# Optimization experiments

Measured on AMD Instinct MI355X. Metric: run time of the kernel, lower is better.

The kernel has to match this reference:

```python
import jax, jax.numpy as jnp
import numpy as np

B, K, T, D, NH, HD, DFF, L = 2, 512, 2048, 1024, 16, 64, 4096, 2
EPS = 1e-5


def rotate_half(x):
    x1, x2 = jnp.split(x, 2, axis=-1)
    return jnp.concatenate([-x2, x1], axis=-1)


def rmsnorm(x, w):
    return x * jax.lax.rsqrt(jnp.mean(x * x, axis=-1, keepdims=True) + EPS) * w


def setup_inputs():
    key = jax.random.key(0)
    ks = jax.random.split(key, 16)
    x_processed = jax.random.normal(ks[0], (B, K, D), jnp.float32)
    # counts[b] = number of chunks n; boundaries[b, :n-1] = ascending chunk ends in (0, T),
    # positions >= n-1 padded with T (sentinel, never used by the original loop).
    counts = jax.random.randint(ks[1], (B,), K // 2, K + 1)
    raw = jnp.sort(jax.random.randint(ks[2], (B, K), 1, T), axis=1)
    j = jnp.arange(K)[None, :]
    boundaries = jnp.where(j < counts[:, None] - 1, raw, T)
    x_residual = jax.random.normal(ks[3], (B, T, D), jnp.float32)
    inv_freq = 1.0 / (10000.0 ** (jnp.arange(0, HD, 2, dtype=jnp.float32) / HD))
    freqs = jnp.arange(T, dtype=jnp.float32)[:, None] * inv_freq[None, :]  # [T, HD//2]
    emb = jnp.concatenate([freqs, freqs], axis=-1)                          # [T, HD]
    cos, sin = jnp.cos(emb), jnp.sin(emb)
    s = 0.02
    wq = jax.random.normal(ks[4], (L, D, D), jnp.float32) * s
    wk = jax.random.normal(ks[5], (L, D, D), jnp.float32) * s
    wv = jax.random.normal(ks[6], (L, D, D), jnp.float32) * s
    wo = jax.random.normal(ks[7], (L, D, D), jnp.float32) * s
    w1 = jax.random.normal(ks[8], (L, D, DFF), jnp.float32) * s
    w3 = jax.random.normal(ks[9], (L, D, DFF), jnp.float32) * s
    w2 = jax.random.normal(ks[10], (L, DFF, D), jnp.float32) * s
    attn_norm_w = jnp.ones((L, D), jnp.float32)
    mlp_norm_w = jnp.ones((L, D), jnp.float32)
    final_norm_w = jnp.ones((D,), jnp.float32)
    return {"x_processed": x_processed, "boundaries": boundaries, "counts": counts,
            "x_residual": x_residual, "cos": cos, "sin": sin, "seq_len": T,
            "wq": wq, "wk": wk, "wv": wv, "wo": wo,
            "attn_norm_w": attn_norm_w, "mlp_norm_w": mlp_norm_w,
            "w1": w1, "w3": w3, "w2": w2, "final_norm_w": final_norm_w}


def reference(x_processed, boundaries, counts, x_residual, cos, sin, seq_len,
              wq, wk, wv, wo, attn_norm_w, mlp_norm_w, w1, w3, w2, final_norm_w):
    Bn, Kn, Dn = x_processed.shape
    Tn = x_residual.shape[1]
    # Vectorized chunk expansion: token t belongs to chunk i = #{boundaries <= t}
    # (boundaries ascending; entries beyond n-1 are padded with seq_len so they never count).
    t = jnp.arange(Tn)
    idx = jax.vmap(lambda row: jnp.searchsorted(row, t, side='right'))(boundaries)  # [B, T]
    x = jnp.take_along_axis(x_processed, idx[:, :, None], axis=1) + x_residual     # [B, T, D]

    mask = jnp.tril(jnp.ones((Tn, Tn), dtype=bool))
    scale = 1.0 / jnp.sqrt(jnp.float32(HD))
    c = cos[None, :, None, :]
    s = sin[None, :, None, :]
    for l in range(L):
        h = rmsnorm(x, attn_norm_w[l])
        q = (h @ wq[l]).reshape(Bn, Tn, NH, HD)
        k = (h @ wk[l]).reshape(Bn, Tn, NH, HD)
        v = (h @ wv[l]).reshape(Bn, Tn, NH, HD)
        q = q * c + rotate_half(q) * s
        k = k * c + rotate_half(k) * s
        scores = jnp.einsum('bthd,bshd->bhts', q, k) * scale
        scores = jnp.where(mask[None, None], scores, -jnp.inf)
        probs = jax.nn.softmax(scores, axis=-1)
        o = jnp.einsum('bhts,bshd->bthd', probs, v).reshape(Bn, Tn, Dn)
        x = x + o @ wo[l]
        h = rmsnorm(x, mlp_norm_w[l])
        x = x + (jax.nn.silu(h @ w1[l]) * (h @ w3[l])) @ w2[l]
    return rmsnorm(x, final_norm_w)
```

## Files before the change

kernel.cpp:

```cpp
#include <hip/hip_runtime.h>
#include <stdint.h>

typedef __attribute__((ext_vector_type(8))) short s16x8;
typedef __attribute__((ext_vector_type(4))) float f32x4;

#define CB 2
#define CT 2048
#define CD 1024
#define CNH 16
#define CHD 64
#define CDFF 4096
#define CKB 512

__device__ __forceinline__ short f2bf(float f){
  union { float f; uint32_t u; } v; v.f = f;
  uint32_t r = v.u + 0x7FFFu + ((v.u >> 16) & 1u);
  return (short)(r >> 16);
}
__device__ __forceinline__ float bf2f(short h){
  union { uint32_t u; float f; } v; v.u = ((uint32_t)(uint16_t)h) << 16;
  return v.f;
}
__device__ __forceinline__ uint32_t cvtpk_bf16(float lo, float hi){
  uint32_t r;
  asm("v_cvt_pk_bf16_f32 %0, %1, %2" : "=v"(r) : "v"(lo), "v"(hi));
  return r;
}

#define GLOAD16(g, l) __builtin_amdgcn_global_load_lds( \
    (const __attribute__((address_space(1))) void*)(g), \
    (__attribute__((address_space(3))) void*)(l), 16, 0, 0)

__global__ void gather_kernel(const float* __restrict__ xp, const int* __restrict__ bnd,
                              const float* __restrict__ xr, float* __restrict__ x){
  int t = blockIdx.x, b = blockIdx.y, tid = threadIdx.x;
  int lo = 0, hi = CKB;
  while (lo < hi){ int mid = (lo + hi) >> 1; if (bnd[b*CKB + mid] <= t) lo = mid + 1; else hi = mid; }
  const float4* s  = (const float4*)(xp + ((size_t)b*CKB + lo)*CD);
  const float4* rr = (const float4*)(xr + ((size_t)b*CT + t)*CD);
  float4* dst      = (float4*)(x  + ((size_t)b*CT + t)*CD);
  float4 a = s[tid], c = rr[tid];
  float4 o; o.x = a.x + c.x; o.y = a.y + c.y; o.z = a.z + c.z; o.w = a.w + c.w;
  dst[tid] = o;
}

__global__ void wtrans_kernel(const float* __restrict__ W, short* __restrict__ dst,
                              int Kd, int Nd){
  __shared__ __align__(16) float tile[64*65];
  int n0 = blockIdx.x*64, k0 = blockIdx.y*64;
  #pragma unroll
  for (int i = 0; i < 16; ++i){
    int e = threadIdx.x + 256*i; int kl = e >> 6, nl = e & 63;
    tile[kl*65 + nl] = W[(size_t)(k0 + kl)*Nd + n0 + nl];
  }
  __syncthreads();
  #pragma unroll
  for (int i = 0; i < 16; ++i){
    int e = threadIdx.x + 256*i; int nl = e >> 6, kl = e & 63;
    dst[(size_t)(n0 + nl)*Kd + k0 + kl] = f2bf(tile[kl*65 + nl]);
  }
}

__global__ void wtrans_inter_kernel(const float* __restrict__ W, short* __restrict__ dst,
                                    int Kd, int Nd, int off16){
  __shared__ __align__(16) float tile[64*65];
  int n0 = blockIdx.x*64, k0 = blockIdx.y*64;
  #pragma unroll
  for (int i = 0; i < 16; ++i){
    int e = threadIdx.x + 256*i; int kl = e >> 6, nl = e & 63;
    tile[kl*65 + nl] = W[(size_t)(k0 + kl)*Nd + n0 + nl];
  }
  __syncthreads();
  #pragma unroll
  for (int i = 0; i < 16; ++i){
    int e = threadIdx.x + 256*i; int nl = e >> 6, kl = e & 63;
    int c = n0 + nl;
    int frow = ((c >> 4) << 5) + off16 + (c & 15);
    dst[(size_t)frow*Kd + k0 + kl] = f2bf(tile[kl*65 + nl]);
  }
}

template<int OUT_BF16>
__global__ void rmsnorm_kernel(const float* __restrict__ x, const float* __restrict__ w,
                               void* __restrict__ outv){
  int row = blockIdx.x, tid = threadIdx.x;
  const float4 xv = ((const float4*)(x + (size_t)row*CD))[tid];
  float ss = xv.x*xv.x + xv.y*xv.y + xv.z*xv.z + xv.w*xv.w;
  #pragma unroll
  for (int m = 1; m < 64; m <<= 1) ss += __shfl_xor(ss, m);
  __shared__ float red[4];
  if ((tid & 63) == 0) red[tid >> 6] = ss;
  __syncthreads();
  float tot = red[0] + red[1] + red[2] + red[3];
  float scale = rsqrtf(tot * (1.0f/1024.0f) + 1e-5f);
  const float4 wv = ((const float4*)w)[tid];
  if (OUT_BF16){
    short4 o;
    o.x = f2bf(xv.x*scale*wv.x); o.y = f2bf(xv.y*scale*wv.y);
    o.z = f2bf(xv.z*scale*wv.z); o.w = f2bf(xv.w*scale*wv.w);
    ((short4*)outv)[(size_t)row*256 + tid] = o;
  } else {
    float4 o;
    o.x = xv.x*scale*wv.x; o.y = xv.y*scale*wv.y;
    o.z = xv.z*scale*wv.z; o.w = xv.w*scale*wv.w;
    ((float4*)outv)[(size_t)row*256 + tid] = o;
  }
}

template<int OUT_BF16>
__global__ void redrms_kernel(float* __restrict__ x, const float* __restrict__ Cp,
                              const float* __restrict__ w, void* __restrict__ outv){
  int row = blockIdx.x, tid = threadIdx.x;
  size_t i = (size_t)row*256 + tid;
  const float4* p0 = (const float4*)Cp;
  const float4* p1 = p0 + (size_t)1048576;
  const float4* p2 = p1 + (size_t)1048576;
  const float4* p3 = p2 + (size_t)1048576;
  float4 a = ((float4*)x)[i];
  float4 q0 = p0[i], q1 = p1[i], q2 = p2[i], q3 = p3[i];
  a.x += (q0.x + q1.x) + (q2.x + q3.x);
  a.y += (q0.y + q1.y) + (q2.y + q3.y);
  a.z += (q0.z + q1.z) + (q2.z + q3.z);
  a.w += (q0.w + q1.w) + (q2.w + q3.w);
  if (OUT_BF16) ((float4*)x)[i] = a;
  float ss = a.x*a.x + a.y*a.y + a.z*a.z + a.w*a.w;
  #pragma unroll
  for (int m = 1; m < 64; m <<= 1) ss += __shfl_xor(ss, m);
  __shared__ float red[4];
  if ((tid & 63) == 0) red[tid >> 6] = ss;
  __syncthreads();
  float tot = red[0] + red[1] + red[2] + red[3];
  float scale = rsqrtf(tot * (1.0f/1024.0f) + 1e-5f);
  const float4 wv = ((const float4*)w)[tid];
  if (OUT_BF16){
    short4 o;
    o.x = f2bf(a.x*scale*wv.x); o.y = f2bf(a.y*scale*wv.y);
    o.z = f2bf(a.z*scale*wv.z); o.w = f2bf(a.w*scale*wv.w);
    ((short4*)outv)[(size_t)row*256 + tid] = o;
  } else {
    float4 o;
    o.x = a.x*scale*wv.x; o.y = a.y*scale*wv.y;
    o.z = a.z*scale*wv.z; o.w = a.w*scale*wv.w;
    ((float4*)outv)[(size_t)row*256 + tid] = o;
  }
}

__device__ __forceinline__ void swz_block_id(int id, int NX, int NY, int& bm, int& bn){
  const int nwg = NX*NY;
  const int qq = nwg >> 3, rr8 = nwg & 7;
  const int xcd = id & 7, loc = id >> 3;
  const int wgid = (xcd < rr8 ? xcd*(qq+1) : rr8*(qq+1) + (xcd-rr8)*qq) + loc;
  const int GM = 8;
  const int gsz = GM * NX;
  const int gidg = wgid / gsz;
  const int remg = wgid - gidg*gsz;
  bm = gidg*GM + (remg % GM);
  bn = remg / GM;
}

template<int EPI>
__global__ __launch_bounds__(256) void gemm_bt(const short* __restrict__ A,
                                               const short* __restrict__ Bt,
                                               void* __restrict__ Cv,
                                               int M, int N, int K,
                                               int NX, int NY){
  __shared__ __align__(16) short sA[2][128*32];
  __shared__ __align__(16) short sB[2][128*32];
  const int tid = threadIdx.x;
  const int lane = tid & 63, wid = tid >> 6;
  const int wm = wid >> 1, wn = wid & 1;
  const int lr = lane & 15, lg = lane >> 4;
  int bm, bn; swz_block_id(blockIdx.x, NX, NY, bm, bn);
  const int bm0 = bm * 128, bn0 = bn * 128;

  f32x4 acc[4][4];
  #pragma unroll
  for (int i = 0; i < 4; ++i)
    #pragma unroll
    for (int j = 0; j < 4; ++j) acc[i][j] = (f32x4){0.f,0.f,0.f,0.f};

  const short* gA = A  + (size_t)(bm0 + wid*32 + (lane >> 2))*K + (lane & 3)*8;
  const short* gB = Bt + (size_t)(bn0 + wid*32 + (lane >> 2))*K + (lane & 3)*8;

  #pragma unroll
  for (int iss = 0; iss < 2; ++iss){
    GLOAD16(gA + (size_t)iss*16*K, &sA[0][wid*1024 + iss*16*32]);
    GLOAD16(gB + (size_t)iss*16*K, &sB[0][wid*1024 + iss*16*32]);
  }
  __syncthreads();

  int cur = 0;
  for (int k0 = 0; k0 < K; k0 += 32){
    if (k0 + 32 < K){
      #pragma unroll
      for (int iss = 0; iss < 2; ++iss){
        GLOAD16(gA + (size_t)iss*16*K + k0 + 32, &sA[cur^1][wid*1024 + iss*16*32]);
        GLOAD16(gB + (size_t)iss*16*K + k0 + 32, &sB[cur^1][wid*1024 + iss*16*32]);
      }
    }
    s16x8 af[4], bq[4];
    #pragma unroll
    for (int i = 0; i < 4; ++i) af[i] = *(const s16x8*)&sA[cur][(wm*64 + i*16 + lr)*32 + lg*8];
    #pragma unroll
    for (int j = 0; j < 4; ++j) bq[j] = *(const s16x8*)&sB[cur][(wn*64 + j*16 + lr)*32 + lg*8];
    #pragma unroll
    for (int i = 0; i < 4; ++i)
      #pragma unroll
      for (int j = 0; j < 4; ++j)
        acc[i][j] = __builtin_amdgcn_mfma_f32_16x16x32_bf16(af[i], bq[j], acc[i][j], 0, 0, 0);
    __syncthreads();
    cur ^= 1;
  }

  if (EPI == 0){
    short* C = (short*)Cv;
    #pragma unroll
    for (int i = 0; i < 4; ++i){
      int row0 = bm0 + wm*64 + i*16 + lg*4;
      #pragma unroll
      for (int j = 0; j < 4; ++j){
        int col = bn0 + wn*64 + j*16 + lr;
        #pragma unroll
        for (int r = 0; r < 4; ++r) C[(size_t)(row0 + r)*N + col] = f2bf(acc[i][j][r]);
      }
    }
  } else {
    float* C = (float*)Cv;
    #pragma unroll
    for (int i = 0; i < 4; ++i){
      int row0 = bm0 + wm*64 + i*16 + lg*4;
      #pragma unroll
      for (int j = 0; j < 4; ++j){
        int col = bn0 + wn*64 + j*16 + lr;
        #pragma unroll
        for (int r = 0; r < 4; ++r) C[(size_t)(row0 + r)*N + col] += acc[i][j][r];
      }
    }
  }
}

#define STAGE8(u, kt, bufx) do { \
  const short* Gp_ = ((u)&1) ? Bt : A; \
  const int rb_ = ((u)&1) ? bn0 : bm0; \
  const int kh_ = (u)>>1; \
  _Pragma("unroll") \
  for (int L_ = 0; L_ < 2; ++L_){ \
    int rowS_ = L_*128 + wid*16 + (lane>>2); \
    int sp_ = (lane&3) ^ ((rowS_>>1)&3); \
    GLOAD16(Gp_ + (size_t)(rb_ + rowS_)*Kstr + (size_t)(kt)*64 + kh_*32 + sp_*8, \
            &sAB[bufx][u][(L_*512 + wid*64)*8]); \
  } \
} while(0)

#define LDSRD(bufx, u, rowv) \
  (*(const s16x8*)&sAB[bufx][u][(rowv)*32 + (((lg) ^ (((rowv)>>1)&3))<<3)])

#define PHASEPAIR(kk) do { \
  if (pf){ STAGE8(2*(kk), kt+1, nbuf); STAGE8(2*(kk)+1, kt+1, nbuf); } \
  s16x8 af0_[4], af1_[4], bq_[4]; \
  _Pragma("unroll") \
  for (int j_ = 0; j_ < 4; ++j_) bq_[j_] = LDSRD(buf, (kk)*2+1, wn*64 + j_*16 + lr); \
  _Pragma("unroll") \
  for (int i_ = 0; i_ < 4; ++i_) af0_[i_] = LDSRD(buf, (kk)*2, wm*128 + i_*16 + lr); \
  _Pragma("unroll") \
  for (int i_ = 0; i_ < 4; ++i_) af1_[i_] = LDSRD(buf, (kk)*2, wm*128 + 64 + i_*16 + lr); \
  __builtin_amdgcn_s_barrier(); \
  asm volatile("s_waitcnt lgkmcnt(0)" ::: "memory"); \
  __builtin_amdgcn_s_setprio(1); \
  _Pragma("unroll") \
  for (int i_ = 0; i_ < 4; ++i_) \
    _Pragma("unroll") \
    for (int j_ = 0; j_ < 4; ++j_) \
      acc[i_][j_] = __builtin_amdgcn_mfma_f32_16x16x32_bf16(af0_[i_], bq_[j_], acc[i_][j_], 0, 0, 0); \
  _Pragma("unroll") \
  for (int i_ = 0; i_ < 4; ++i_) \
    _Pragma("unroll") \
    for (int j_ = 0; j_ < 4; ++j_) \
      acc[4+i_][j_] = __builtin_amdgcn_mfma_f32_16x16x32_bf16(af1_[i_], bq_[j_], acc[4+i_][j_], 0, 0, 0); \
  __builtin_amdgcn_s_setprio(0); \
  if (pf) asm volatile("s_waitcnt vmcnt(4)" ::: "memory"); \
  else if ((kk) == 0) asm volatile("s_waitcnt vmcnt(0)" ::: "memory"); \
  __builtin_amdgcn_s_barrier(); \
} while(0)

template<int FUSE>
__global__ __launch_bounds__(512, 2) void gemm8p(const short* __restrict__ A,
                                                 const short* __restrict__ Bt,
                                                 void* __restrict__ Cv,
                                                 short* __restrict__ Qo,
                                                 short* __restrict__ Ko,
                                                 short* __restrict__ Vo,
                                                 const float* __restrict__ cosb,
                                                 const float* __restrict__ sinb,
                                                 int M, int N, int Kstr, int Kchunk,
                                                 int NX, int NY){
  __shared__ __align__(16) short sAB[2][4][256*32];
  const int tid = threadIdx.x;
  const int lane = tid & 63, wid = tid >> 6;
  const int wm = wid >> 2, wn = wid & 3;
  const int lr = lane & 15, lg = lane >> 4;
  const int nin = NX*NY;
  const int split = blockIdx.x / nin;
  const int inner = blockIdx.x - split*nin;
  int bm, bn; swz_block_id(inner, NX, NY, bm, bn);
  const int bm0 = bm * 256, bn0 = bn * 256;
  A  += (size_t)split * Kchunk;
  Bt += (size_t)split * Kchunk;

  f32x4 acc[8][4];
  #pragma unroll
  for (int i = 0; i < 8; ++i)
    #pragma unroll
    for (int j = 0; j < 4; ++j) acc[i][j] = (f32x4){0.f,0.f,0.f,0.f};

  const int NK = Kchunk >> 6;
  STAGE8(0, 0, 0);
  STAGE8(1, 0, 0);
  STAGE8(2, 0, 0);
  STAGE8(3, 0, 0);
  asm volatile("s_waitcnt vmcnt(4)" ::: "memory");
  __builtin_amdgcn_s_barrier();

  #pragma unroll 1
  for (int kt = 0; kt < NK; ++kt){
    const bool pf = (kt + 1 < NK);
    const int buf = kt & 1, nbuf = buf ^ 1;
    PHASEPAIR(0);
    PHASEPAIR(1);
  }

  if (FUSE == 0){
    short* C = (short*)Cv;
    #pragma unroll
    for (int i = 0; i < 8; ++i){
      int row0 = bm0 + wm*128 + i*16 + lg*4;
      #pragma unroll
      for (int j = 0; j < 4; ++j){
        int col = bn0 + wn*64 + j*16 + lr;
        #pragma unroll
        for (int r = 0; r < 4; ++r) C[(size_t)(row0 + r)*N + col] = f2bf(acc[i][j][r]);
      }
    }
  } else if (FUSE == 1){
    short* C = (short*)Cv;
    const int Nh = N >> 1;
    #pragma unroll
    for (int i = 0; i < 8; ++i){
      int row0 = bm0 + wm*128 + i*16 + lg*4;
      #pragma unroll
      for (int jp = 0; jp < 2; ++jp){
        int col = (bn0 >> 1) + wn*32 + jp*16 + lr;
        #pragma unroll
        for (int r = 0; r < 4; ++r){
          float u = acc[i][jp*2][r], g = acc[i][jp*2+1][r];
          float val = u / (1.f + __expf(-u)) * g;
          C[(size_t)(row0 + r)*Nh + col] = f2bf(val);
        }
      }
    }
  } else if (FUSE == 2){
    float* C = (float*)Cv + (size_t)split*M*N;
    #pragma unroll
    for (int i = 0; i < 8; ++i){
      int row0 = bm0 + wm*128 + i*16 + lg*4;
      #pragma unroll
      for (int j = 0; j < 4; ++j){
        int col = bn0 + wn*64 + j*16 + lr;
        #pragma unroll
        for (int r = 0; r < 4; ++r) C[(size_t)(row0 + r)*N + col] = acc[i][j][r];
      }
    }
  } else {
    const int part = bn0 >> 10;
    const int colb = bn0 & 1023;
    const int h = (colb + wn*64) >> 6;
    if (part < 2){
      short* dst = (part == 0) ? Qo : Ko;
      const float qs = (part == 0) ? 0.1803368801111204f : 1.0f;
      #pragma unroll
      for (int i = 0; i < 8; ++i){
        int row0 = bm0 + wm*128 + i*16 + lg*4;
        #pragma unroll
        for (int jh = 0; jh < 2; ++jh){
          int d = jh*16 + lr;
          #pragma unroll
          for (int r = 0; r < 4; ++r){
            int tg = row0 + r;
            int bb = tg >> 11, tt = tg & 2047;
            float c = cosb[tt*64 + d], s = sinb[tt*64 + d];
            float x0 = acc[i][jh][r], x1 = acc[i][jh+2][r];
            float y0 = (x0*c - x1*s)*qs;
            float y1 = (x1*c + x0*s)*qs;
            size_t o = ((size_t)(bb*CT + tt)*CNH + h)*CHD;
            dst[o + d]      = f2bf(y0);
            dst[o + d + 32] = f2bf(y1);
          }
        }
      }
    } else {
      #pragma unroll
      for (int i = 0; i < 8; ++i){
        int row0 = bm0 + wm*128 + i*16 + lg*4;
        int bb = row0 >> 11, t0 = row0 & 2047;
        #pragma unroll
        for (int j = 0; j < 4; ++j){
          int d = j*16 + lr;
          short4 pk;
          pk.x = f2bf(acc[i][j][0]); pk.y = f2bf(acc[i][j][1]);
          pk.z = f2bf(acc[i][j][2]); pk.w = f2bf(acc[i][j][3]);
          *(short4*)&Vo[((size_t)(bb*CNH + h)*CHD + d)*CT + t0] = pk;
        }
      }
    }
  }
}

__global__ __launch_bounds__(256) void attn_kernel(const short* __restrict__ Q,
                                                   const short* __restrict__ Kb,
                                                   const short* __restrict__ Vt,
                                                   short* __restrict__ O){
  __shared__ __align__(16) short Kl[2][64*72];
  __shared__ __align__(16) short Vl[2][64*72];
  __shared__ __align__(16) short Pl[4][16*72];
  const int tid = threadIdx.x, lane = tid & 63, w = tid >> 6;
  const int qpair = blockIdx.x;
  const int h = blockIdx.y, b = blockIdx.z;
  const int lr = lane & 15, lg = lane >> 4;

  const short* gK = Kb + (size_t)b*CT*CD + h*CHD;
  const short* gV = Vt + (size_t)(b*CNH + h)*CHD*CT;
  const int srow0 = tid >> 3, scol = (tid & 7)*8;

  #pragma unroll 1
  for (int half = 0; half < 2; ++half){
    const int qt = half ? qpair : (31 - qpair);
    const int wq0 = qt*64 + w*16;
    const int jmax = qt + 1;

    s16x8 qf0, qf1;
    {
      const short* qp = Q + ((size_t)(b*CT + wq0 + lr)*CNH + h)*CHD + lg*8;
      qf0 = *(const s16x8*)qp;
      qf1 = *(const s16x8*)(qp + 32);
    }
    f32x4 oacc[4];
    #pragma unroll
    for (int dt = 0; dt < 4; ++dt) oacc[dt] = (f32x4){0.f,0.f,0.f,0.f};
    float m_r = -1e30f, l_r = 0.f;

    #pragma unroll
    for (int p = 0; p < 2; ++p){
      int row = srow0 + p*32;
      *(s16x8*)&Kl[0][row*72 + scol] = *(const s16x8*)(gK + (size_t)row*CD + scol);
      *(s16x8*)&Vl[0][row*72 + scol] = *(const s16x8*)(gV + (size_t)row*CT + scol);
    }
    __syncthreads();

    #pragma unroll 1
    for (int j = 0; j < jmax; ++j){
      const int kv0 = j*64;
      const int buf = j & 1;
      s16x8 nk[2], nv[2];
      const bool havenext = (j + 1 < jmax);
      if (havenext){
        const int kv1 = kv0 + 64;
        #pragma unroll
        for (int p = 0; p < 2; ++p){
          int row = srow0 + p*32;
          nk[p] = *(const s16x8*)(gK + (size_t)(kv1 + row)*CD + scol);
          nv[p] = *(const s16x8*)(gV + (size_t)row*CT + kv1 + scol);
        }
      }

      if (kv0 < wq0 + 16){
        f32x4 sc[4];
        __builtin_amdgcn_s_setprio(1);
        #pragma unroll
        for (int nt = 0; nt < 4; ++nt){
          s16x8 k0 = *(const s16x8*)&Kl[buf][(nt*16 + lr)*72 + lg*8];
          s16x8 k1 = *(const s16x8*)&Kl[buf][(nt*16 + lr)*72 + 32 + lg*8];
          f32x4 z = (f32x4){0.f,0.f,0.f,0.f};
          z = __builtin_amdgcn_mfma_f32_16x16x32_bf16(k0, qf0, z, 0, 0, 0);
          z = __builtin_amdgcn_mfma_f32_16x16x32_bf16(k1, qf1, z, 0, 0, 0);
          sc[nt] = z;
        }
        __builtin_amdgcn_s_setprio(0);
        if (kv0 + 64 > wq0){
          #pragma unroll
          for (int nt = 0; nt < 4; ++nt)
            #pragma unroll
            for (int r = 0; r < 4; ++r)
              if (kv0 + nt*16 + lg*4 + r > wq0 + lr) sc[nt][r] = -1e30f;
        }
        float pmax = sc[0][0];
        #pragma unroll
        for (int nt = 0; nt < 4; ++nt)
          #pragma unroll
          for (int r = 0; r < 4; ++r) pmax = fmaxf(pmax, sc[nt][r]);
        pmax = fmaxf(pmax, __shfl_xor(pmax, 16));
        pmax = fmaxf(pmax, __shfl_xor(pmax, 32));
        if (!__all(pmax - m_r <= 10.f)){
          float mn = fmaxf(m_r, pmax);
          float corr = __builtin_amdgcn_exp2f(m_r - mn);
          m_r = mn;
          l_r *= corr;
          #pragma unroll
          for (int r = 0; r < 4; ++r){
            float c4 = __shfl(corr, lg*4 + r);
            #pragma unroll
            for (int dt = 0; dt < 4; ++dt) oacc[dt][r] *= c4;
          }
        }
        float rs = 0.f;
        #pragma unroll
        for (int nt = 0; nt < 4; ++nt)
          #pragma unroll
          for (int r = 0; r < 4; ++r){
            float pv = __builtin_amdgcn_exp2f(sc[nt][r] - m_r);
            sc[nt][r] = pv;
            rs += pv;
          }
        #pragma unroll
        for (int nt = 0; nt < 4; ++nt){
          uint2 pk;
          pk.x = cvtpk_bf16(sc[nt][0], sc[nt][1]);
          pk.y = cvtpk_bf16(sc[nt][2], sc[nt][3]);
          *(uint2*)&Pl[w][lr*72 + nt*16 + lg*4] = pk;
        }
        rs += __shfl_xor(rs, 16);
        rs += __shfl_xor(rs, 32);
        l_r += rs;
        s16x8 pa0 = *(const s16x8*)&Pl[w][lr*72 + lg*8];
        s16x8 pa1 = *(const s16x8*)&Pl[w][lr*72 + 32 + lg*8];
        __builtin_amdgcn_s_setprio(1);
        #pragma unroll
        for (int dt = 0; dt < 4; ++dt){
          s16x8 v0 = *(const s16x8*)&Vl[buf][(dt*16 + lr)*72 + lg*8];
          s16x8 v1 = *(const s16x8*)&Vl[buf][(dt*16 + lr)*72 + 32 + lg*8];
          oacc[dt] = __builtin_amdgcn_mfma_f32_16x16x32_bf16(pa0, v0, oacc[dt], 0, 0, 0);
          oacc[dt] = __builtin_amdgcn_mfma_f32_16x16x32_bf16(pa1, v1, oacc[dt], 0, 0, 0);
        }
        __builtin_amdgcn_s_setprio(0);
      }
      if (havenext){
        #pragma unroll
        for (int p = 0; p < 2; ++p){
          int row = srow0 + p*32;
          *(s16x8*)&Kl[buf^1][row*72 + scol] = nk[p];
          *(s16x8*)&Vl[buf^1][row*72 + scol] = nv[p];
        }
      }
      __syncthreads();
    }

    #pragma unroll
    for (int r = 0; r < 4; ++r){
      float lf = __shfl(l_r, lg*4 + r);
      float inv = 1.f / lf;
      int qrow = wq0 + lg*4 + r;
      #pragma unroll
      for (int dt = 0; dt < 4; ++dt)
        O[((size_t)(b*CT + qrow)*CNH + h)*CHD + dt*16 + lr] = f2bf(oacc[dt][r] * inv);
    }
  }
}

extern "C" void kernel_launch(void* const* d_in, const int* in_sizes, int n_in,
                              void* d_out, int out_size, void* d_ws, size_t ws_size,
                              hipStream_t stream){
  (void)in_sizes; (void)n_in; (void)out_size; (void)ws_size;
  const float* x_processed = (const float*)d_in[0];
  const int*   boundaries  = (const int*)d_in[1];
  const float* x_residual  = (const float*)d_in[3];
  const float* cosb        = (const float*)d_in[4];
  const float* sinb        = (const float*)d_in[5];
  const float* wq          = (const float*)d_in[7];
  const float* wk          = (const float*)d_in[8];
  const float* wv          = (const float*)d_in[9];
  const float* wo          = (const float*)d_in[10];
  const float* attn_nw     = (const float*)d_in[11];
  const float* mlp_nw      = (const float*)d_in[12];
  const float* w1          = (const float*)d_in[13];
  const float* w3          = (const float*)d_in[14];
  const float* w2          = (const float*)d_in[15];
  const float* final_nw    = (const float*)d_in[16];

  char* p = (char*)d_ws;
  auto alloc = [&](size_t bytes)->char*{
    char* r = p; p += (bytes + 255) & ~(size_t)255; return r;
  };
  short* wqkvT = (short*)alloc((size_t)2*3072*1024*2);
  short* woT   = (short*)alloc((size_t)2*1024*1024*2);
  short* w13T  = (short*)alloc((size_t)2*8192*1024*2);
  short* w2T   = (short*)alloc((size_t)2*1024*4096*2);
  float* x     = (float*)alloc((size_t)4096*1024*4);
  short* hbuf  = (short*)alloc((size_t)4096*1024*2);
  short* qr    = (short*)alloc((size_t)4096*1024*2);
  short* kr    = (short*)alloc((size_t)4096*1024*2);
  short* vt    = (short*)alloc((size_t)4096*1024*2);
  short* obuf  = (short*)alloc((size_t)4096*1024*2);
  short* mbuf  = (short*)alloc((size_t)4096*4096*2);
  float* psum  = (float*)alloc((size_t)4*4096*1024*4);

  for (int l = 0; l < 2; ++l){
    size_t wOff = (size_t)l*1024*1024;
    wtrans_kernel<<<dim3(16,16),256,0,stream>>>(wq + wOff, wqkvT + (size_t)l*3072*1024,                     1024, 1024);
    wtrans_kernel<<<dim3(16,16),256,0,stream>>>(wk + wOff, wqkvT + (size_t)l*3072*1024 + (size_t)1024*1024, 1024, 1024);
    wtrans_kernel<<<dim3(16,16),256,0,stream>>>(wv + wOff, wqkvT + (size_t)l*3072*1024 + (size_t)2048*1024, 1024, 1024);
    wtrans_kernel<<<dim3(16,16),256,0,stream>>>(wo + wOff, woT + (size_t)l*1024*1024,                       1024, 1024);
    wtrans_inter_kernel<<<dim3(64,16),256,0,stream>>>(w1 + (size_t)l*1024*4096, w13T + (size_t)l*8192*1024, 1024, 4096, 0);
    wtrans_inter_kernel<<<dim3(64,16),256,0,stream>>>(w3 + (size_t)l*1024*4096, w13T + (size_t)l*8192*1024, 1024, 4096, 16);
    wtrans_kernel<<<dim3(16,64),256,0,stream>>>(w2 + (size_t)l*4096*1024, w2T + (size_t)l*1024*4096,        4096, 1024);
  }
  gather_kernel<<<dim3(2048,2),256,0,stream>>>(x_processed, boundaries, x_residual, x);
  rmsnorm_kernel<1><<<4096,256,0,stream>>>(x, attn_nw, hbuf);
  for (int l = 0; l < 2; ++l){
    gemm8p<3><<<12*16,512,0,stream>>>(hbuf, wqkvT + (size_t)l*3072*1024, nullptr,
                                      qr, kr, vt, cosb, sinb,
                                      4096, 3072, 1024, 1024, 12, 16);
    attn_kernel<<<dim3(16,16,2),256,0,stream>>>(qr, kr, vt, obuf);
    gemm_bt<1><<<8*32,256,0,stream>>>(obuf, woT + (size_t)l*1024*1024, x, 4096, 1024, 1024, 8, 32);
    rmsnorm_kernel<1><<<4096,256,0,stream>>>(x, mlp_nw + l*1024, hbuf);
    gemm8p<1><<<32*16,512,0,stream>>>(hbuf, w13T + (size_t)l*8192*1024, mbuf,
                                      nullptr, nullptr, nullptr, nullptr, nullptr,
                                      4096, 8192, 1024, 1024, 32, 16);
    gemm8p<2><<<4*4*16,512,0,stream>>>(mbuf, w2T + (size_t)l*1024*4096, psum,
                                       nullptr, nullptr, nullptr, nullptr, nullptr,
                                       4096, 1024, 4096, 1024, 4, 16);
    if (l == 0) redrms_kernel<1><<<4096,256,0,stream>>>(x, psum, attn_nw + 1024, hbuf);
    else        redrms_kernel<0><<<4096,256,0,stream>>>(x, psum, final_nw, d_out);
  }
}
```

Measured before the change: 607.6 us.

## Deepen gemm8p prefetch to two k-tiles and merge weight-transpose launches

The main GEMM loop is reorganized into four quarter-phases that issue global-to-LDS loads two k-tiles ahead instead of one. It reuses the A fragments across two B-column halves with finer vmcnt waits, aiming to hide more memory latency behind MFMA work. The per-layer weight-transpose launches are also merged into fewer kernels using blockIdx.z to select the matrix, cutting launch overhead. The deeper prefetch writes into the buffer currently being read, so its correctness depends on the barrier and vmcnt ordering, and it adds register pressure from holding eight A fragments.

Result: faster. 584.1 us (-3.9%).

```diff
diff --git a/kernel.cpp b/kernel.cpp
--- a/kernel.cpp
+++ b/kernel.cpp
@@ -44,6 +44,30 @@
   dst[tid] = o;
 }
 
+__global__ void wtrans_qkvo_kernel(const float* __restrict__ wq, const float* __restrict__ wk,
+                                   const float* __restrict__ wv, const float* __restrict__ wo,
+                                   short* __restrict__ qkvT, short* __restrict__ woT){
+  __shared__ __align__(16) float tile[64*65];
+  const float* W; short* dst;
+  const int z = blockIdx.z;
+  if (z == 0){ W = wq; dst = qkvT; }
+  else if (z == 1){ W = wk; dst = qkvT + (size_t)1024*1024; }
+  else if (z == 2){ W = wv; dst = qkvT + (size_t)2048*1024; }
+  else { W = wo; dst = woT; }
+  int n0 = blockIdx.x*64, k0 = blockIdx.y*64;
+  #pragma unroll
+  for (int i = 0; i < 16; ++i){
+    int e = threadIdx.x + 256*i; int kl = e >> 6, nl = e & 63;
+    tile[kl*65 + nl] = W[(size_t)(k0 + kl)*1024 + n0 + nl];
+  }
+  __syncthreads();
+  #pragma unroll
+  for (int i = 0; i < 16; ++i){
+    int e = threadIdx.x + 256*i; int nl = e >> 6, kl = e & 63;
+    dst[(size_t)(n0 + nl)*1024 + k0 + kl] = f2bf(tile[kl*65 + nl]);
+  }
+}
+
 __global__ void wtrans_kernel(const float* __restrict__ W, short* __restrict__ dst,
                               int Kd, int Nd){
   __shared__ __align__(16) float tile[64*65];
@@ -61,14 +85,16 @@
   }
 }
 
-__global__ void wtrans_inter_kernel(const float* __restrict__ W, short* __restrict__ dst,
-                                    int Kd, int Nd, int off16){
+__global__ void wtrans_inter2_kernel(const float* __restrict__ w1p, const float* __restrict__ w3p,
+                                     short* __restrict__ dst){
   __shared__ __align__(16) float tile[64*65];
+  const float* W = blockIdx.z ? w3p : w1p;
+  const int off16 = blockIdx.z ? 16 : 0;
   int n0 = blockIdx.x*64, k0 = blockIdx.y*64;
   #pragma unroll
   for (int i = 0; i < 16; ++i){
     int e = threadIdx.x + 256*i; int kl = e >> 6, nl = e & 63;
-    tile[kl*65 + nl] = W[(size_t)(k0 + kl)*Nd + n0 + nl];
+    tile[kl*65 + nl] = W[(size_t)(k0 + kl)*4096 + n0 + nl];
   }
   __syncthreads();
   #pragma unroll
@@ -76,7 +102,7 @@
     int e = threadIdx.x + 256*i; int nl = e >> 6, kl = e & 63;
     int c = n0 + nl;
     int frow = ((c >> 4) << 5) + off16 + (c & 15);
-    dst[(size_t)frow*Kd + k0 + kl] = f2bf(tile[kl*65 + nl]);
+    dst[(size_t)frow*1024 + k0 + kl] = f2bf(tile[kl*65 + nl]);
   }
 }
 
@@ -254,34 +280,6 @@
 
 #define LDSRD(bufx, u, rowv) \
   (*(const s16x8*)&sAB[bufx][u][(rowv)*32 + (((lg) ^ (((rowv)>>1)&3))<<3)])
-
-#define PHASEPAIR(kk) do { \
-  if (pf){ STAGE8(2*(kk), kt+1, nbuf); STAGE8(2*(kk)+1, kt+1, nbuf); } \
-  s16x8 af0_[4], af1_[4], bq_[4]; \
-  _Pragma("unroll") \
-  for (int j_ = 0; j_ < 4; ++j_) bq_[j_] = LDSRD(buf, (kk)*2+1, wn*64 + j_*16 + lr); \
-  _Pragma("unroll") \
-  for (int i_ = 0; i_ < 4; ++i_) af0_[i_] = LDSRD(buf, (kk)*2, wm*128 + i_*16 + lr); \
-  _Pragma("unroll") \
-  for (int i_ = 0; i_ < 4; ++i_) af1_[i_] = LDSRD(buf, (kk)*2, wm*128 + 64 + i_*16 + lr); \
-  __builtin_amdgcn_s_barrier(); \
-  asm volatile("s_waitcnt lgkmcnt(0)" ::: "memory"); \
-  __builtin_amdgcn_s_setprio(1); \
-  _Pragma("unroll") \
-  for (int i_ = 0; i_ < 4; ++i_) \
-    _Pragma("unroll") \
-    for (int j_ = 0; j_ < 4; ++j_) \
-      acc[i_][j_] = __builtin_amdgcn_mfma_f32_16x16x32_bf16(af0_[i_], bq_[j_], acc[i_][j_], 0, 0, 0); \
-  _Pragma("unroll") \
-  for (int i_ = 0; i_ < 4; ++i_) \
-    _Pragma("unroll") \
-    for (int j_ = 0; j_ < 4; ++j_) \
-      acc[4+i_][j_] = __builtin_amdgcn_mfma_f32_16x16x32_bf16(af1_[i_], bq_[j_], acc[4+i_][j_], 0, 0, 0); \
-  __builtin_amdgcn_s_setprio(0); \
-  if (pf) asm volatile("s_waitcnt vmcnt(4)" ::: "memory"); \
-  else if ((kk) == 0) asm volatile("s_waitcnt vmcnt(0)" ::: "memory"); \
-  __builtin_amdgcn_s_barrier(); \
-} while(0)
 
 template<int FUSE>
 __global__ __launch_bounds__(512, 2) void gemm8p(const short* __restrict__ A,
@@ -314,19 +312,91 @@
     for (int j = 0; j < 4; ++j) acc[i][j] = (f32x4){0.f,0.f,0.f,0.f};
 
   const int NK = Kchunk >> 6;
-  STAGE8(0, 0, 0);
-  STAGE8(1, 0, 0);
-  STAGE8(2, 0, 0);
-  STAGE8(3, 0, 0);
-  asm volatile("s_waitcnt vmcnt(4)" ::: "memory");
+  STAGE8(0, 0, 0); STAGE8(1, 0, 0); STAGE8(2, 0, 0); STAGE8(3, 0, 0);
+  if (NK > 1){
+    STAGE8(0, 1, 1); STAGE8(1, 1, 1); STAGE8(2, 1, 1);
+    asm volatile("s_waitcnt vmcnt(10)" ::: "memory");
+  } else {
+    asm volatile("s_waitcnt vmcnt(4)" ::: "memory");
+  }
   __builtin_amdgcn_s_barrier();
 
+  s16x8 afp[8];
   #pragma unroll 1
   for (int kt = 0; kt < NK; ++kt){
-    const bool pf = (kt + 1 < NK);
-    const int buf = kt & 1, nbuf = buf ^ 1;
-    PHASEPAIR(0);
-    PHASEPAIR(1);
+    const int cur = kt & 1, nxt = cur ^ 1;
+    const bool st1 = (kt + 1 < NK);
+    const bool st2 = (kt + 2 < NK);
+
+    if (st1) STAGE8(3, kt+1, nxt);
+    {
+      #pragma unroll
+      for (int i_ = 0; i_ < 8; ++i_) afp[i_] = LDSRD(cur, 0, wm*128 + i_*16 + lr);
+      s16x8 b0 = LDSRD(cur, 1, wn*64 + lr);
+      s16x8 b1 = LDSRD(cur, 1, wn*64 + 16 + lr);
+      __builtin_amdgcn_s_barrier();
+      asm volatile("s_waitcnt lgkmcnt(0)" ::: "memory");
+      __builtin_amdgcn_s_setprio(1);
+      #pragma unroll
+      for (int i_ = 0; i_ < 8; ++i_){
+        acc[i_][0] = __builtin_amdgcn_mfma_f32_16x16x32_bf16(afp[i_], b0, acc[i_][0], 0, 0, 0);
+        acc[i_][1] = __builtin_amdgcn_mfma_f32_16x16x32_bf16(afp[i_], b1, acc[i_][1], 0, 0, 0);
+      }
+      __builtin_amdgcn_s_setprio(0);
+      __builtin_amdgcn_s_barrier();
+    }
+    if (st2) STAGE8(0, kt+2, cur);
+    {
+      s16x8 b2 = LDSRD(cur, 1, wn*64 + 32 + lr);
+      s16x8 b3 = LDSRD(cur, 1, wn*64 + 48 + lr);
+      __builtin_amdgcn_s_barrier();
+      asm volatile("s_waitcnt lgkmcnt(0)" ::: "memory");
+      __builtin_amdgcn_s_setprio(1);
+      #pragma unroll
+      for (int i_ = 0; i_ < 8; ++i_){
+        acc[i_][2] = __builtin_amdgcn_mfma_f32_16x16x32_bf16(afp[i_], b2, acc[i_][2], 0, 0, 0);
+        acc[i_][3] = __builtin_amdgcn_mfma_f32_16x16x32_bf16(afp[i_], b3, acc[i_][3], 0, 0, 0);
+      }
+      __builtin_amdgcn_s_setprio(0);
+      if (st2)      asm volatile("s_waitcnt vmcnt(10)" ::: "memory");
+      else if (st1) asm volatile("s_waitcnt vmcnt(8)"  ::: "memory");
+      else          asm volatile("s_waitcnt vmcnt(0)"  ::: "memory");
+      __builtin_amdgcn_s_barrier();
+    }
+    if (st2) STAGE8(1, kt+2, cur);
+    {
+      #pragma unroll
+      for (int i_ = 0; i_ < 8; ++i_) afp[i_] = LDSRD(cur, 2, wm*128 + i_*16 + lr);
+      s16x8 b0 = LDSRD(cur, 3, wn*64 + lr);
+      s16x8 b1 = LDSRD(cur, 3, wn*64 + 16 + lr);
+      __builtin_amdgcn_s_barrier();
+      asm volatile("s_waitcnt lgkmcnt(0)" ::: "memory");
+      __builtin_amdgcn_s_setprio(1);
+      #pragma unroll
+      for (int i_ = 0; i_ < 8; ++i_){
+        acc[i_][0] = __builtin_amdgcn_mfma_f32_16x16x32_bf16(afp[i_], b0, acc[i_][0], 0, 0, 0);
+        acc[i_][1] = __builtin_amdgcn_mfma_f32_16x16x32_bf16(afp[i_], b1, acc[i_][1], 0, 0, 0);
+      }
+      __builtin_amdgcn_s_setprio(0);
+      __builtin_amdgcn_s_barrier();
+    }
+    if (st2) STAGE8(2, kt+2, cur);
+    {
+      s16x8 b2 = LDSRD(cur, 3, wn*64 + 32 + lr);
+      s16x8 b3 = LDSRD(cur, 3, wn*64 + 48 + lr);
+      __builtin_amdgcn_s_barrier();
+      asm volatile("s_waitcnt lgkmcnt(0)" ::: "memory");
+      __builtin_amdgcn_s_setprio(1);
+      #pragma unroll
+      for (int i_ = 0; i_ < 8; ++i_){
+        acc[i_][2] = __builtin_amdgcn_mfma_f32_16x16x32_bf16(afp[i_], b2, acc[i_][2], 0, 0, 0);
+        acc[i_][3] = __builtin_amdgcn_mfma_f32_16x16x32_bf16(afp[i_], b3, acc[i_][3], 0, 0, 0);
+      }
+      __builtin_amdgcn_s_setprio(0);
+      if (st2)      asm volatile("s_waitcnt vmcnt(10)" ::: "memory");
+      else if (st1) asm volatile("s_waitcnt vmcnt(4)"  ::: "memory");
+      __builtin_amdgcn_s_barrier();
+    }
   }
 
   if (FUSE == 0){
@@ -604,13 +674,11 @@
 
   for (int l = 0; l < 2; ++l){
     size_t wOff = (size_t)l*1024*1024;
-    wtrans_kernel<<<dim3(16,16),256,0,stream>>>(wq + wOff, wqkvT + (size_t)l*3072*1024,                     1024, 1024);
-    wtrans_kernel<<<dim3(16,16),256,0,stream>>>(wk + wOff, wqkvT + (size_t)l*3072*1024 + (size_t)1024*1024, 1024, 1024);
-    wtrans_kernel<<<dim3(16,16),256,0,stream>>>(wv + wOff, wqkvT + (size_t)l*3072*1024 + (size_t)2048*1024, 1024, 1024);
-    wtrans_kernel<<<dim3(16,16),256,0,stream>>>(wo + wOff, woT + (size_t)l*1024*1024,                       1024, 1024);
-    wtrans_inter_kernel<<<dim3(64,16),256,0,stream>>>(w1 + (size_t)l*1024*4096, w13T + (size_t)l*8192*1024, 1024, 4096, 0);
-    wtrans_inter_kernel<<<dim3(64,16),256,0,stream>>>(w3 + (size_t)l*1024*4096, w13T + (size_t)l*8192*1024, 1024, 4096, 16);
-    wtrans_kernel<<<dim3(16,64),256,0,stream>>>(w2 + (size_t)l*4096*1024, w2T + (size_t)l*1024*4096,        4096, 1024);
+    wtrans_qkvo_kernel<<<dim3(16,16,4),256,0,stream>>>(wq + wOff, wk + wOff, wv + wOff, wo + wOff,
+                                                       wqkvT + (size_t)l*3072*1024, woT + (size_t)l*1024*1024);
+    wtrans_inter2_kernel<<<dim3(64,16,2),256,0,stream>>>(w1 + (size_t)l*1024*4096, w3 + (size_t)l*1024*4096,
+                                                         w13T + (size_t)l*8192*1024);
+    wtrans_kernel<<<dim3(16,64),256,0,stream>>>(w2 + (size_t)l*4096*1024, w2T + (size_t)l*1024*4096, 4096, 1024);
   }
   gather_kernel<<<dim3(2048,2),256,0,stream>>>(x_processed, boundaries, x_residual, x);
   rmsnorm_kernel<1><<<4096,256,0,stream>>>(x, attn_nw, hbuf);
```
